# Kernel tuning notes

Measured on AMD Instinct MI355X. Metric: run time of the kernel, lower is better.

## Reference

```python
import jax, jax.numpy as jnp
import numpy as np
from jax import lax

NK = 21   # num_kernels / predicted kernel size
MK = 21   # max_kernel_size
B, H, W = 8, 256, 256


def _make_gauss_weight():
    """Fixed bank: identity kernel + 21 FFT-inverse gaussian kernels, repeated x3 channels."""
    def gauss1d(ws, sigma):
        xs = np.arange(ws)
        g = np.exp(-(xs - ws // 2) ** 2 / (2.0 * sigma ** 2))
        return g / g.sum()

    def inv_kernel(ws, sigma):
        g = gauss1d(ws, sigma)
        w2 = np.outer(g, g)
        K = np.fft.fft2(w2)
        K = np.conj(K) / (np.abs(K) ** 2 + 0.01)
        return np.abs(np.fft.ifft2(K))

    w = np.zeros((NK + 1, 1, MK, MK), np.float32)
    ks = 3
    for i in range(NK):
        pad = (MK - ks) // 2
        w[i + 1, 0, pad:pad + ks, pad:pad + ks] = inv_kernel(ks, 0.25 * (i + 1))
        if i >= 2 and i % 2 == 0 and ks < MK:
            ks += 2
    w[0, 0, MK // 2, MK // 2] = 1.0  # identity (delta) kernel
    return np.repeat(w, 3, axis=0)   # (66, 1, 21, 21)


def conv(x, w, pad, groups=1, b=None):
    y = lax.conv_general_dilated(
        x, w, (1, 1), [(pad, pad), (pad, pad)],
        dimension_numbers=("NCHW", "OIHW", "NCHW"),
        feature_group_count=groups)
    if b is not None:
        y = y + b[None, :, None, None]
    return y


def adaptive_avg_pool(x, oh, ow):
    """Matches torch AdaptiveAvgPool2d bin boundaries (static shapes)."""
    Hh, Ww = x.shape[2], x.shape[3]
    def bins(L, o):
        return [((i * L) // o, -((-(i + 1) * L) // o)) for i in range(o)]
    rows = []
    for (hs, he) in bins(Hh, oh):
        cols = [x[:, :, hs:he, ws:we].mean(axis=(2, 3)) for (ws, we) in bins(Ww, ow)]
        rows.append(jnp.stack(cols, axis=-1))
    return jnp.stack(rows, axis=-2)  # (N, C, oh, ow)


def setup_inputs() -> dict:
    key = jax.random.key(0)
    ks = jax.random.split(key, 12)
    s = 0.02
    return {
        "x": jax.random.normal(ks[0], (B, 3, H, W), jnp.float32),
        "w_gauss": jnp.asarray(_make_gauss_weight()),
        "p1_w": jax.random.normal(ks[1], (128, 3, 11, 11), jnp.float32) * s,
        "p1_b": jax.random.normal(ks[2], (128,), jnp.float32) * s,
        "p2_w": jax.random.normal(ks[3], (441, 128, 1, 1), jnp.float32) * s,
        "p3_w": jax.random.normal(ks[4], (441, 441, 1, 1), jnp.float32) * s,
        "cs_w": jax.random.normal(ks[5], (3, 3, 3, 3), jnp.float32) * s,
        "cs_b": jax.random.normal(ks[6], (3,), jnp.float32) * s,
        "tr_w": jax.random.normal(ks[7], (66, 3, 3, 3), jnp.float32) * s,
        "tr_b": jax.random.normal(ks[8], (66,), jnp.float32) * s,
        "fu_w": jax.random.normal(ks[9], (66, 132, 3, 3), jnp.float32) * s,
        "fu_b": jax.random.normal(ks[10], (66,), jnp.float32) * s,
    }


def reference(x, w_gauss, p1_w, p1_b, p2_w, p3_w, cs_w, cs_b, tr_w, tr_b, fu_w, fu_b):
    b = x.shape[0]
    pad = (NK - 1) // 2  # 10

    # fixed inverse-gaussian blur bank, grouped over the 3 input channels -> (B,66,H,W)
    x_gauss = conv(x, w_gauss, pad, groups=3)

    # Predictor: per-sample 3x21x21 dynamic kernel
    h = jax.nn.leaky_relu(conv(x, p1_w, 2, b=p1_b), 0.2)
    h = adaptive_avg_pool(h, 3, 3)
    h = jax.nn.leaky_relu(conv(h, p2_w, 0), 0.2)
    h = adaptive_avg_pool(h, 3, 1)           # (B,441,3,1)
    h = jax.nn.softmax(conv(h, p3_w, 0), axis=1)
    kern = h.reshape(b, 3, NK, NK)           # per-sample predicted kernel

    # batched per-sample dynamic conv: groups=B trick replaces the python loop
    xr = x.reshape(1, b * 3, x.shape[2], x.shape[3])
    out = conv(xr, kern, pad, groups=b)      # (1,B,H,W)
    output = jnp.broadcast_to(out.reshape(b, 1, x.shape[2], x.shape[3]), x.shape)

    ax_out = conv(x, cs_w, 1, b=cs_b)                       # (B,3,H,W)
    x_af = conv(output, tr_w, 1, b=tr_b)                    # (B,66,H,W)
    fused = conv(jnp.concatenate([x_gauss, x_af], axis=1), fu_w, 1, b=fu_b)  # (B,66,H,W)
    return (fused, ax_out)
```

## Files before the change

### kernel.cpp

```cpp
#include <hip/hip_runtime.h>
#include <hip/hip_bf16.h>

#define BB 8
#define HH 256
#define WW 256
#define HW 65536

typedef __attribute__((ext_vector_type(8))) short bf16x8;
typedef __attribute__((ext_vector_type(4))) float f32x4;
typedef __attribute__((ext_vector_type(8))) unsigned short u16x8;
#define MFMA16(a, b, c) __builtin_amdgcn_mfma_f32_16x16x32_bf16(a, b, c, 0, 0, 0)

__device__ __forceinline__ ushort f2bf(float f) {
  union { float f; uint32_t u; } c; c.f = f;
  uint32_t r = (c.u + 0x7fffu + ((c.u >> 16) & 1u)) >> 16;
  return (ushort)r;
}

#define OFF_XG    0
#define OFF_PP    25165824
#define OFF_XGN   69206016
#define OFF_OUT1  144703488
#define OFF_KERN  146837504
#define OFF_BW    146880000
#define OFF_BWZ   147018240
#define OFF_BP    147028480
#define OFF_BIAS  147126784
#define OFF_TB    147127296
#define OFF_T     147129856

__global__ __launch_bounds__(256) void k_prepA(const float* __restrict__ fuw,
                                               const float* __restrict__ trw,
                                               const float* __restrict__ trb,
                                               const float* __restrict__ p1w,
                                               float* __restrict__ T,
                                               float* __restrict__ TB,
                                               ushort* __restrict__ Bw,
                                               ushort* __restrict__ Bp) {
  int i = blockIdx.x * 256 + threadIdx.x;
  if (i < 5346) {
    int o = i / 81, a = (i / 9) % 9, s = i % 9;
    float acc = 0.f;
    for (int cp = 0; cp < 66; ++cp)
      acc += fuw[(o * 132 + 66 + cp) * 9 + a] *
             (trw[(cp * 3) * 9 + s] + trw[(cp * 3 + 1) * 9 + s] + trw[(cp * 3 + 2) * 9 + s]);
    T[i] = acc; return;
  }
  i -= 5346;
  if (i < 594) {
    int o = i / 9, a = i % 9;
    float acc = 0.f;
    for (int cp = 0; cp < 66; ++cp) acc += trb[cp] * fuw[(o * 132 + 66 + cp) * 9 + a];
    TB[i] = acc; return;
  }
  i -= 594;
  if (i < 2 * 9 * 80 * 32) {
    int cc = i / 23040, t = (i / 2560) % 9, o = (i / 32) % 80, kl = i & 31;
    int c = cc * 32 + kl;
    Bw[i] = (o < 66) ? f2bf(fuw[(o * 132 + c) * 9 + t]) : 0;
    return;
  }
  i -= 2 * 9 * 80 * 32;
  if (i < 12 * 128 * 32) {
    int kc = i / 4096, o = (i / 32) % 128, kl = i & 31;
    int k = kc * 32 + kl;
    float v = 0.f;
    if (k < 363) { int u = k / 33, r2 = k % 33, vv = r2 / 3, c = r2 % 3;
                   v = p1w[(o * 3 + c) * 121 + u * 11 + vv]; }
    Bp[i] = f2bf(v);
    return;
  }
}

__device__ __forceinline__ float W5val(int o, int d, const float* T) {
  int dy = d / 5, dx = d % 5;
  float acc = 0.f;
  for (int ua = 0; ua < 3; ++ua) {
    int us = dy - ua; if (us < 0 || us > 2) continue;
    for (int va = 0; va < 3; ++va) {
      int vs = dx - va; if (vs < 0 || vs > 2) continue;
      acc += T[(o * 9 + ua * 3 + va) * 9 + us * 3 + vs];
    }
  }
  return acc;
}

__global__ __launch_bounds__(256) void k_prepB(const float* __restrict__ fuw,
                                               const float* __restrict__ fub,
                                               const float* __restrict__ T,
                                               const float* __restrict__ TB,
                                               ushort* __restrict__ BwZ,
                                               float* __restrict__ bias_tot) {
  int i = blockIdx.x * 256 + threadIdx.x;
  if (i < 5120) {
    int zc = i / 2560, o = (i / 32) % 80, s = i & 31;
    float v = 0.f;
    if (o < 66) {
      if (zc == 0) {
        if (s < 18) { int ch = 64 + s / 9, a = s % 9; v = fuw[(o * 132 + ch) * 9 + a]; }
        else        { v = W5val(o, s - 18, T); }
      } else {
        if (s < 11) v = W5val(o, 14 + s, T);
      }
    }
    BwZ[i] = f2bf(v); return;
  }
  i -= 5120;
  if (i < 80) {
    float v = 0.f;
    if (i < 66) { v = fub[i]; for (int a = 0; a < 9; ++a) v += TB[i * 9 + a]; }
    bias_tot[i] = v;
  }
}

template <int KS>
__device__ __forceinline__ void xg_conv(const float* __restrict__ xt,
                                        const float* __restrict__ wgp,
                                        float* a, int r, int wq) {
  constexpr int P0 = (21 - KS) / 2;
  constexpr int Q0 = P0 & ~3;
  constexpr int D0 = P0 - Q0;
  constexpr int NL = ((P0 + KS + 6) >> 2) - (P0 >> 2) + 1;
#pragma unroll 1
  for (int kh = P0; kh < P0 + KS; ++kh) {
    float rx[NL * 4];
    const int F0 = (r + kh) * 320 + 8 * wq + Q0;
#pragma unroll
    for (int i = 0; i < NL; ++i) {
      int Fi = F0 + 4 * i;
      *(float4*)(rx + 4 * i) = *(const float4*)(xt + (Fi ^ (((Fi >> 5) & 1) << 2)));
    }
    const float* wr = wgp + kh * 21 + P0;
#pragma unroll
    for (int t = 0; t < KS; ++t) {
      float wv = wr[t];
#pragma unroll
      for (int u = 0; u < 8; ++u) a[u] += wv * rx[D0 + t + u];
    }
  }
}

__global__ __launch_bounds__(256, 4) void k_xgauss(const float* __restrict__ x,
                                                   const float* __restrict__ wg,
                                                   __hip_bfloat16* __restrict__ xg) {
  const int bu = blockIdx.z;
  const int b = bu / 24, u = bu % 24;
  const int g = u >> 3;
  const int j = (u & 7) + 7 * g;
  const int h0 = blockIdx.y * 8;
  __shared__ __align__(16) float xt[28 * 320];
  const float* xp = x + (b * 3 + g) * HW;
  for (int e = threadIdx.x; e < 28 * 320; e += 256) {
    int row = e / 320, col = e % 320;
    int gy = h0 + row - 10, gx = col - 10;
    float v = (gy >= 0 && gy < HH && gx >= 0 && gx < WW) ? xp[gy * WW + gx] : 0.f;
    xt[e ^ (((e >> 5) & 1) << 2)] = v;
  }
  __syncthreads();
  int i_ = j - 1;
  int im = (i_ - 1 > 0) ? (i_ - 1) : 0;
  const int ks = (j == 0) ? 1 : 3 + 2 * (im >> 1);
  const int wq = threadIdx.x & 31, r = threadIdx.x >> 5;
  const float* wgp = wg + (3 * j) * 441;
  float a[8] = {0.f, 0.f, 0.f, 0.f, 0.f, 0.f, 0.f, 0.f};
  switch (ks) {
    case 1:  xg_conv<1>(xt, wgp, a, r, wq); break;
    case 3:  xg_conv<3>(xt, wgp, a, r, wq); break;
    case 5:  xg_conv<5>(xt, wgp, a, r, wq); break;
    case 7:  xg_conv<7>(xt, wgp, a, r, wq); break;
    case 9:  xg_conv<9>(xt, wgp, a, r, wq); break;
    case 11: xg_conv<11>(xt, wgp, a, r, wq); break;
    case 13: xg_conv<13>(xt, wgp, a, r, wq); break;
    case 15: xg_conv<15>(xt, wgp, a, r, wq); break;
    case 17: xg_conv<17>(xt, wgp, a, r, wq); break;
    case 19: xg_conv<19>(xt, wgp, a, r, wq); break;
    default: xg_conv<21>(xt, wgp, a, r, wq); break;
  }
  u16x8 ov;
#pragma unroll
  for (int k = 0; k < 8; ++k) ov[k] = f2bf(a[k]);
  int oidx = (bu * HW) + (h0 + r) * WW + 8 * wq;
  *(u16x8*)((ushort*)xg + oidx) = ov;
}

__global__ __launch_bounds__(256) void k_tr(const ushort* __restrict__ xg,
                                            ushort* __restrict__ xgn) {
  __shared__ ushort ls[64 * 72];
  int p0 = blockIdx.x * 64;
  int b = p0 >> 16, sp = p0 & 65535;
  for (int e = threadIdx.x; e < 72 * 64; e += 256) {
    int c = e >> 6, i = e & 63;
    int uc = c / 3 + c / 22;
    ls[i * 72 + c] = (c < 66) ? xg[(size_t)(b * 24 + uc) * HW + sp + i] : (ushort)0;
  }
  __syncthreads();
  for (int e = threadIdx.x; e < 576; e += 256) {
    *(float4*)(xgn + (size_t)p0 * 72 + e * 8) = *(const float4*)(ls + e * 8);
  }
}

__global__ __launch_bounds__(256, 2) void k_pmm(const float* __restrict__ x,
                                                const ushort* __restrict__ Bp,
                                                const float* __restrict__ p1b,
                                                float* __restrict__ pp) {
  __shared__ float xt[26 * 26 * 3];
  __shared__ float ps[1152];
  const int b = blockIdx.z, h0 = blockIdx.y * 16, w0 = blockIdx.x * 16;
  const int tid = threadIdx.x, wave = tid >> 6, lane = tid & 63;
  const int m = lane & 15, q = lane >> 4;
  for (int e = tid; e < 1152; e += 256) ps[e] = 0.f;
  for (int e = tid; e < 676; e += 256) {
    int py = e / 26, pxc = e % 26, gy = h0 - 2 + py, gx = w0 - 2 + pxc;
    bool in = (gy >= 0 && gy < HH && gx >= 0 && gx < WW);
#pragma unroll
    for (int c = 0; c < 3; ++c)
      xt[e * 3 + c] = in ? x[(b * 3 + c) * HW + gy * WW + gx] : 0.f;
  }
  f32x4 acc[4][8];
#pragma unroll
  for (int a = 0; a < 4; ++a)
#pragma unroll
    for (int n = 0; n < 8; ++n) acc[a][n] = (f32x4){0.f, 0.f, 0.f, 0.f};
  __syncthreads();
  const int q8 = q * 8;
#pragma unroll
  for (int kc = 0; kc < 12; ++kc) {
    bf16x8 bf[8];
#pragma unroll
    for (int nt = 0; nt < 8; ++nt)
      bf[nt] = *(const bf16x8*)(Bp + ((kc * 128 + nt * 16 + m) * 32 + q8));
    int off[8];
#pragma unroll
    for (int j = 0; j < 8; ++j) {
      int k = kc * 32 + q8 + j;
      int kk = (kc == 11) ? (k > 362 ? 362 : k) : k;
      off[j] = kk + (kk / 33) * 45;
    }
#pragma unroll
    for (int mt = 0; mt < 4; ++mt) {
      const int row = (wave << 2) + mt;
      const int pb = (row * 26 + m) * 3;
      union { ushort us[8]; bf16x8 v; } af;
#pragma unroll
      for (int j = 0; j < 8; ++j) {
        ushort bvv = f2bf(xt[pb + off[j]]);
        if (kc == 11) {
          int k = kc * 32 + q8 + j;
          bvv = (k < 363) ? bvv : (ushort)0;
        }
        af.us[j] = bvv;
      }
#pragma unroll
      for (int nt = 0; nt < 8; ++nt)
        acc[mt][nt] = MFMA16(af.v, bf[nt], acc[mt][nt]);
    }
  }
  float bv[8];
#pragma unroll
  for (int nt = 0; nt < 8; ++nt) bv[nt] = p1b[nt * 16 + m];
#pragma unroll
  for (int mt = 0; mt < 4; ++mt) {
    int h = h0 + (wave << 2) + mt;
    if (h >= 250) continue;
    bool h0m = h < 84, h1m = (h >= 83 && h < 167), h2m = h >= 166;
#pragma unroll
    for (int r = 0; r < 4; ++r) {
      int w = w0 + (q << 2) + r;
      if (w >= 250) continue;
      bool w0m = w < 84, w1m = (w >= 83 && w < 167), w2m = w >= 166;
#pragma unroll
      for (int nt = 0; nt < 8; ++nt) {
        int o = (nt << 4) + m;
        float vz = acc[mt][nt][r] + bv[nt];
        vz = vz >= 0.f ? vz : 0.2f * vz;
        if (h0m) { if (w0m) atomicAdd(&ps[o], vz);        if (w1m) atomicAdd(&ps[128 + o], vz);
                   if (w2m) atomicAdd(&ps[256 + o], vz); }
        if (h1m) { if (w0m) atomicAdd(&ps[384 + o], vz);  if (w1m) atomicAdd(&ps[512 + o], vz);
                   if (w2m) atomicAdd(&ps[640 + o], vz); }
        if (h2m) { if (w0m) atomicAdd(&ps[768 + o], vz);  if (w1m) atomicAdd(&ps[896 + o], vz);
                   if (w2m) atomicAdd(&ps[1024 + o], vz); }
      }
    }
  }
  __syncthreads();
  const int tile = blockIdx.y * 16 + blockIdx.x;
  float* dst = pp + (size_t)(b * 256 + tile) * 1152;
  for (int e = tid; e < 1152; e += 256)
    dst[e] = ps[(e % 9) * 128 + (e / 9)];
}

__global__ __launch_bounds__(256) void k_pred2(const float* __restrict__ pp,
                                               const float* __restrict__ p2w,
                                               const float* __restrict__ p3w,
                                               float* __restrict__ kernw) {
  const int b = blockIdx.x;
  const int tid = threadIdx.x;
  __shared__ float hin[1152];
  __shared__ float h2p[1323];
  __shared__ float h3l[1323];
  __shared__ float mx[3], sm[3];
  for (int e = tid; e < 1152; e += 256) {
    float s = 0.f;
    const float* qp = pp + (size_t)b * 256 * 1152 + e;
#pragma unroll 4
    for (int t = 0; t < 256; ++t) s += qp[t * 1152];
    hin[e] = s * (1.f / 7056.f);
  }
  __syncthreads();
  for (int c = tid; c < 441; c += 256) {
    float z[9] = {0.f,0.f,0.f,0.f,0.f,0.f,0.f,0.f,0.f};
    const float* wr = p2w + c * 128;
    for (int k = 0; k < 128; k++) {
      float wv = wr[k];
      const float* hp = &hin[k * 9];
#pragma unroll
      for (int p = 0; p < 9; p++) z[p] += wv * hp[p];
    }
#pragma unroll
    for (int i = 0; i < 3; i++) {
      float s = 0.f;
#pragma unroll
      for (int jj = 0; jj < 3; jj++) {
        float zz = z[i * 3 + jj];
        s += (zz >= 0.f) ? zz : 0.2f * zz;
      }
      h2p[c * 3 + i] = s * (1.f / 3.f);
    }
  }
  __syncthreads();
  for (int c = tid; c < 441; c += 256) {
    float a0 = 0.f, a1 = 0.f, a2 = 0.f;
    const float* wr = p3w + c * 441;
    for (int k = 0; k < 441; k++) {
      float wv = wr[k];
      a0 += wv * h2p[k * 3];
      a1 += wv * h2p[k * 3 + 1];
      a2 += wv * h2p[k * 3 + 2];
    }
    h3l[c * 3] = a0; h3l[c * 3 + 1] = a1; h3l[c * 3 + 2] = a2;
  }
  __syncthreads();
  if (tid < 3) {
    float mxv = -1e30f;
    for (int c = 0; c < 441; c++) mxv = fmaxf(mxv, h3l[c * 3 + tid]);
    float s = 0.f;
    for (int c = 0; c < 441; c++) s += expf(h3l[c * 3 + tid] - mxv);
    mx[tid] = mxv; sm[tid] = 1.f / s;
  }
  __syncthreads();
  for (int f = tid; f < 1323; f += 256) {
    int i = f % 3;
    kernw[b * 1323 + f] = expf(h3l[f] - mx[i]) * sm[i];
  }
}

__global__ __launch_bounds__(256) void k_dyn(const float* __restrict__ x,
                                             const float* __restrict__ kernw,
                                             float* __restrict__ out1) {
  const int b = blockIdx.z;
  const int h0 = blockIdx.y * 16, w0 = blockIdx.x * 64;
  __shared__ float kl[1323];
  __shared__ float xt[3 * 36 * 84];
  for (int e = threadIdx.x; e < 1323; e += 256) kl[e] = kernw[b * 1323 + e];
  for (int e = threadIdx.x; e < 3 * 36 * 84; e += 256) {
    int ci = e / 3024, rem = e % 3024;
    int ty = rem / 84, tx = rem % 84;
    int gy = h0 + ty - 10, gx = w0 + tx - 10;
    xt[e] = (gy >= 0 && gy < HH && gx >= 0 && gx < WW)
                ? x[(b * 3 + ci) * HW + gy * WW + gx] : 0.f;
  }
  __syncthreads();
  const int wq = threadIdx.x & 15, r = threadIdx.x >> 4;
  float a0 = 0.f, a1 = 0.f, a2 = 0.f, a3 = 0.f;
  for (int ci = 0; ci < 3; ci++) {
    for (int kh = 0; kh < 21; kh++) {
      float rx[24];
      const float4* rp = (const float4*)&xt[ci * 3024 + (r + kh) * 84 + 4 * wq];
      float4* rv = (float4*)rx;
#pragma unroll
      for (int i = 0; i < 6; i++) rv[i] = rp[i];
      const float* wr = &kl[ci * 441 + kh * 21];
#pragma unroll
      for (int kw = 0; kw < 21; kw++) {
        float wv = wr[kw];
        a0 += wv * rx[kw];     a1 += wv * rx[kw + 1];
        a2 += wv * rx[kw + 2]; a3 += wv * rx[kw + 3];
      }
    }
  }
  int idx = b * HW + (h0 + r) * WW + w0 + 4 * wq;
  *(float4*)&out1[idx] = make_float4(a0, a1, a2, a3);
}

__global__ __launch_bounds__(256) void k_ax(const float* __restrict__ x,
                                            const float* __restrict__ csw,
                                            const float* __restrict__ csb,
                                            float* __restrict__ out2) {
  int idx = blockIdx.x * 256 + threadIdx.x;
  if (idx >= BB * 3 * HW) return;
  int w = idx & 255, h = (idx >> 8) & 255;
  int oc = (idx >> 16) % 3, b = idx / (3 * HW);
  float acc = csb[oc];
  for (int ic = 0; ic < 3; ic++) {
    const float* xc = x + (b * 3 + ic) * HW;
    const float* wp = csw + (oc * 3 + ic) * 9;
#pragma unroll
    for (int u = 0; u < 3; u++) {
      int iy = h + u - 1;
      if (iy < 0 || iy >= HH) continue;
#pragma unroll
      for (int v = 0; v < 3; v++) {
        int ix = w + v - 1;
        if (ix >= 0 && ix < WW) acc += xc[iy * WW + ix] * wp[u * 3 + v];
      }
    }
  }
  out2[idx] = acc;
}

__global__ __launch_bounds__(256, 3) void k_fmma(const ushort* __restrict__ xgn,
                                                 const float* __restrict__ out1,
                                                 const ushort* __restrict__ Bw,
                                                 const ushort* __restrict__ BwZ,
                                                 const float* __restrict__ bias_tot,
                                                 float* __restrict__ outf) {
  __shared__ __align__(16) char smem[40080];
  ushort* xs  = (ushort*)smem;
  float*  o1s = (float*)(smem + 20736);
  ushort* xs2 = (ushort*)(smem + 22336);
  ushort* az  = (ushort*)(smem + 23632);
  float*  st  = (float*)(smem + 23632);
  const int b = blockIdx.z, h0 = blockIdx.y * 16, w0 = blockIdx.x * 16;
  const int tid = threadIdx.x, wave = tid >> 6, lane = tid & 63;
  const int m = lane & 15, q = lane >> 4;
  f32x4 acc[4][5];
#pragma unroll
  for (int a = 0; a < 4; ++a)
#pragma unroll
    for (int n = 0; n < 5; ++n) acc[a][n] = (f32x4){0.f, 0.f, 0.f, 0.f};

  for (int cc = 0; cc < 2; ++cc) {
    __syncthreads();
    for (int e = tid; e < 1296; e += 256) {
      int u = e & 3, p = e >> 2, py = p / 18, px = p % 18;
      int gy = h0 - 1 + py, gx = w0 - 1 + px;
      float4 v = make_float4(0.f, 0.f, 0.f, 0.f);
      if (gy >= 0 && gy < HH && gx >= 0 && gx < WW)
        v = *(const float4*)(xgn + (size_t)(b * HW + gy * WW + gx) * 72 + cc * 32 + u * 8);
      *(float4*)(xs + p * 32 + u * 8) = v;
    }
    __syncthreads();
#pragma unroll
    for (int t = 0; t < 9; ++t) {
      const int u = t / 3, v = t % 3;
      bf16x8 bf[5];
#pragma unroll
      for (int nt = 0; nt < 5; ++nt)
        bf[nt] = *(const bf16x8*)(Bw + (((cc * 9 + t) * 80 + nt * 16 + m) * 32 + q * 8));
#pragma unroll
      for (int mt = 0; mt < 4; ++mt) {
        int row = (wave << 2) + mt;
        bf16x8 af = *(const bf16x8*)(xs + ((row + u) * 18 + m + v) * 32 + q * 8);
#pragma unroll
        for (int nt = 0; nt < 5; ++nt)
          acc[mt][nt] = MFMA16(af, bf[nt], acc[mt][nt]);
      }
    }
  }
  __syncthreads();
  for (int e = tid; e < 324; e += 256) {
    int py = e / 18, px = e % 18, gy = h0 - 1 + py, gx = w0 - 1 + px;
    uint32_t v = 0;
    if (gy >= 0 && gy < HH && gx >= 0 && gx < WW)
      v = *(const uint32_t*)(xgn + (size_t)(b * HW + gy * WW + gx) * 72 + 64);
    *(uint32_t*)(xs2 + e * 2) = v;
  }
  for (int e = tid; e < 400; e += 256) {
    int py = e / 20, px = e % 20, gy = h0 - 2 + py, gx = w0 - 2 + px;
    o1s[e] = (gy >= 0 && gy < HH && gx >= 0 && gx < WW) ? out1[b * HW + gy * WW + gx] : 0.f;
  }
  __syncthreads();
  const int bpy = tid >> 4, bpx = tid & 15;
#pragma unroll
  for (int zc = 0; zc < 2; ++zc) {
    union { ushort us[32]; float4 f4[4]; } vals;
    if (zc == 0) {
#pragma unroll
      for (int s = 0; s < 18; ++s) {
        int ch = s / 9, a = s % 9, u = a / 3, v = a % 3;
        vals.us[s] = xs2[((bpy + u) * 18 + bpx + v) * 2 + ch];
      }
#pragma unroll
      for (int d = 0; d < 14; ++d)
        vals.us[18 + d] = f2bf(o1s[(bpy + d / 5) * 20 + bpx + d % 5]);
    } else {
#pragma unroll
      for (int s = 0; s < 11; ++s) {
        int d = 14 + s;
        vals.us[s] = f2bf(o1s[(bpy + d / 5) * 20 + bpx + d % 5]);
      }
#pragma unroll
      for (int s = 11; s < 32; ++s) vals.us[s] = 0;
    }
    __syncthreads();
#pragma unroll
    for (int u = 0; u < 4; ++u)
      *(float4*)(az + tid * 32 + ((u ^ (tid & 3)) << 3)) = vals.f4[u];
    __syncthreads();
    bf16x8 bf[5];
#pragma unroll
    for (int nt = 0; nt < 5; ++nt)
      bf[nt] = *(const bf16x8*)(BwZ + ((zc * 80 + nt * 16 + m) * 32 + q * 8));
#pragma unroll
    for (int mt = 0; mt < 4; ++mt) {
      int px = (((wave << 2) + mt) << 4) + m;
      bf16x8 af = *(const bf16x8*)(az + px * 32 + ((q ^ (px & 3)) << 3));
#pragma unroll
      for (int nt = 0; nt < 5; ++nt)
        acc[mt][nt] = MFMA16(af, bf[nt], acc[mt][nt]);
    }
  }
#pragma unroll 1
  for (int nt = 0; nt < 5; ++nt) {
    __syncthreads();
#pragma unroll
    for (int mt = 0; mt < 4; ++mt) {
      int pxb = (((wave << 2) + mt) << 4);
#pragma unroll
      for (int r = 0; r < 4; ++r)
        st[m * 257 + pxb + q * 4 + r] = acc[mt][nt][r];
    }
    __syncthreads();
#pragma unroll
    for (int kk = 0; kk < 16; ++kk) {
      int o = nt * 16 + kk;
      if (o < 66) {
        float bvv = bias_tot[o];
        outf[((b * 66 + o) * HH + h0 + (tid >> 4)) * WW + w0 + (tid & 15)] =
            st[kk * 257 + tid] + bvv;
      }
    }
  }
}

__global__ __launch_bounds__(256) void k_fix(const float* __restrict__ out1,
                                             const float* __restrict__ T,
                                             const float* __restrict__ TB,
                                             float* __restrict__ outf) {
  int idx = blockIdx.x * 256 + threadIdx.x;
  if (idx >= 8 * 1020 * 66) return;
  int b = idx / (1020 * 66);
  int rem = idx % (1020 * 66);
  int pi = rem / 66, o = rem % 66;
  int ph, pw;
  if (pi < 256)      { ph = 0;        pw = pi; }
  else if (pi < 512) { ph = 255;      pw = pi - 256; }
  else if (pi < 766) { ph = pi - 511; pw = 0; }
  else               { ph = pi - 765; pw = 255; }
  float corr = 0.f;
#pragma unroll
  for (int a = 0; a < 9; ++a) {
    int ua = a / 3, va = a % 3;
    int qh = ph + ua - 1, qw = pw + va - 1;
    if (qh >= 0 && qh < HH && qw >= 0 && qw < WW) continue;
    float s = TB[o * 9 + a];
#pragma unroll
    for (int t2 = 0; t2 < 9; ++t2) {
      int rh = qh + t2 / 3 - 1, rw = qw + t2 % 3 - 1;
      if (rh >= 0 && rh < HH && rw >= 0 && rw < WW)
        s += out1[b * HW + rh * WW + rw] * T[(o * 9 + a) * 9 + t2];
    }
    corr += s;
  }
  outf[((b * 66 + o) * HH + ph) * WW + pw] -= corr;
}

extern "C" void kernel_launch(void* const* d_in, const int* in_sizes, int n_in,
                              void* d_out, int out_size, void* d_ws, size_t ws_size,
                              hipStream_t stream) {
  const float* x   = (const float*)d_in[0];
  const float* wg  = (const float*)d_in[1];
  const float* p1w = (const float*)d_in[2];
  const float* p1b = (const float*)d_in[3];
  const float* p2w = (const float*)d_in[4];
  const float* p3w = (const float*)d_in[5];
  const float* csw = (const float*)d_in[6];
  const float* csb = (const float*)d_in[7];
  const float* trw = (const float*)d_in[8];
  const float* trb = (const float*)d_in[9];
  const float* fuw = (const float*)d_in[10];
  const float* fub = (const float*)d_in[11];
  float* outf = (float*)d_out;
  float* out2 = outf + 34603008;
  char* ws = (char*)d_ws;
  __hip_bfloat16* xg = (__hip_bfloat16*)(ws + OFF_XG);
  float* pp      = (float*)(ws + OFF_PP);
  ushort* xgn    = (ushort*)(ws + OFF_XGN);
  float* out1    = (float*)(ws + OFF_OUT1);
  float* kernw   = (float*)(ws + OFF_KERN);
  ushort* Bw     = (ushort*)(ws + OFF_BW);
  ushort* BwZ    = (ushort*)(ws + OFF_BWZ);
  ushort* Bp     = (ushort*)(ws + OFF_BP);
  float* biasT   = (float*)(ws + OFF_BIAS);
  float* TBp     = (float*)(ws + OFF_TB);
  float* Tp      = (float*)(ws + OFF_T);

  hipLaunchKernelGGL(k_prepA, dim3(397), dim3(256), 0, stream,
                     fuw, trw, trb, p1w, Tp, TBp, Bw, Bp);
  hipLaunchKernelGGL(k_prepB, dim3(21), dim3(256), 0, stream,
                     fuw, fub, Tp, TBp, BwZ, biasT);
  hipLaunchKernelGGL(k_xgauss, dim3(1, 32, 8 * 24), dim3(256), 0, stream, x, wg, xg);
  hipLaunchKernelGGL(k_tr, dim3(8192), dim3(256), 0, stream, (const ushort*)xg, xgn);
  hipLaunchKernelGGL(k_pmm, dim3(16, 16, 8), dim3(256), 0, stream, x, Bp, p1b, pp);
  hipLaunchKernelGGL(k_pred2, dim3(8), dim3(256), 0, stream, pp, p2w, p3w, kernw);
  hipLaunchKernelGGL(k_dyn, dim3(4, 16, 8), dim3(256), 0, stream, x, kernw, out1);
  hipLaunchKernelGGL(k_fmma, dim3(16, 16, 8), dim3(256), 0, stream,
                     xgn, out1, Bw, BwZ, biasT, outf);
  hipLaunchKernelGGL(k_fix, dim3(2104), dim3(256), 0, stream, out1, Tp, TBp, outf);
  hipLaunchKernelGGL(k_ax, dim3(6144), dim3(256), 0, stream, x, csw, csb, out2);
}
```

Baseline: 1.335 ms.

## Pad predictor conv im2col to 4-channel layout and quadruple k_pmm threads

Stores the k_pmm input tile with 4 channels per pixel (the fourth zero) and re-lays out the 11x11 weight matrix to K=484. Each A fragment can then be read with two float4 LDS loads instead of eight scalar gathers with index arithmetic. The block grows to 1024 threads with one 16-pixel row per wave, and shared-memory atomics are spread across four per-quad partial buffers that are summed at the end. This adds about 33% more MFMA work for the zero padding and changes occupancy and register pressure.

```diff
diff --git a/kernel.cpp b/kernel.cpp
--- a/kernel.cpp
+++ b/kernel.cpp
@@ -19,12 +19,12 @@
 
 #define OFF_XG    0
 #define OFF_PP    25165824
+#define OFF_BP    34603008
 #define OFF_XGN   69206016
 #define OFF_OUT1  144703488
 #define OFF_KERN  146837504
 #define OFF_BW    146880000
 #define OFF_BWZ   147018240
-#define OFF_BP    147028480
 #define OFF_BIAS  147126784
 #define OFF_TB    147127296
 #define OFF_T     147129856
@@ -61,12 +61,12 @@
     return;
   }
   i -= 2 * 9 * 80 * 32;
-  if (i < 12 * 128 * 32) {
+  if (i < 16 * 128 * 32) {
     int kc = i / 4096, o = (i / 32) % 128, kl = i & 31;
     int k = kc * 32 + kl;
     float v = 0.f;
-    if (k < 363) { int u = k / 33, r2 = k % 33, vv = r2 / 3, c = r2 % 3;
-                   v = p1w[(o * 3 + c) * 121 + u * 11 + vv]; }
+    if (k < 484) { int u = k / 44, r2 = k % 44, vv = r2 / 4, c = r2 & 3;
+                   if (c < 3) v = p1w[(o * 3 + c) * 121 + u * 11 + vv]; }
     Bp[i] = f2bf(v);
     return;
   }
@@ -199,69 +199,60 @@
   }
 }
 
-__global__ __launch_bounds__(256, 2) void k_pmm(const float* __restrict__ x,
-                                                const ushort* __restrict__ Bp,
-                                                const float* __restrict__ p1b,
-                                                float* __restrict__ pp) {
-  __shared__ float xt[26 * 26 * 3];
-  __shared__ float ps[1152];
+__global__ __launch_bounds__(1024, 4) void k_pmm(const float* __restrict__ x,
+                                                 const ushort* __restrict__ Bp,
+                                                 const float* __restrict__ p1b,
+                                                 float* __restrict__ pp) {
+  __shared__ __align__(16) float xt2[3840];
+  __shared__ float ps[4 * 1152];
   const int b = blockIdx.z, h0 = blockIdx.y * 16, w0 = blockIdx.x * 16;
   const int tid = threadIdx.x, wave = tid >> 6, lane = tid & 63;
   const int m = lane & 15, q = lane >> 4;
-  for (int e = tid; e < 1152; e += 256) ps[e] = 0.f;
-  for (int e = tid; e < 676; e += 256) {
-    int py = e / 26, pxc = e % 26, gy = h0 - 2 + py, gx = w0 - 2 + pxc;
-    bool in = (gy >= 0 && gy < HH && gx >= 0 && gx < WW);
-#pragma unroll
-    for (int c = 0; c < 3; ++c)
-      xt[e * 3 + c] = in ? x[(b * 3 + c) * HW + gy * WW + gx] : 0.f;
-  }
-  f32x4 acc[4][8];
-#pragma unroll
-  for (int a = 0; a < 4; ++a)
-#pragma unroll
-    for (int n = 0; n < 8; ++n) acc[a][n] = (f32x4){0.f, 0.f, 0.f, 0.f};
+  for (int e = tid; e < 4608; e += 1024) ps[e] = 0.f;
+  if (tid < 676) {
+    int py = tid / 26, pxc = tid % 26, gy = h0 - 2 + py, gx = w0 - 2 + pxc;
+    float4 v = make_float4(0.f, 0.f, 0.f, 0.f);
+    if (gy >= 0 && gy < HH && gx >= 0 && gx < WW) {
+      const float* xb = x + b * 3 * HW + gy * WW + gx;
+      v.x = xb[0]; v.y = xb[HW]; v.z = xb[2 * HW];
+    }
+    *(float4*)(xt2 + tid * 4) = v;
+  }
+  for (int e = tid; e < 1136; e += 1024) xt2[2704 + e] = 0.f;
+  f32x4 acc[8];
+#pragma unroll
+  for (int n = 0; n < 8; ++n) acc[n] = (f32x4){0.f, 0.f, 0.f, 0.f};
   __syncthreads();
   const int q8 = q * 8;
-#pragma unroll
-  for (int kc = 0; kc < 12; ++kc) {
+  const float* afb = xt2 + (wave * 26 + m) * 4;
+#pragma unroll
+  for (int kc = 0; kc < 16; ++kc) {
+    const int s = kc * 32 + q8;
+    const int u = (s * 745) >> 15;
+    const int rem = s - 44 * u;
+    const int a0 = s + 60 * u;
+    const int a1 = a0 + ((rem == 40) ? 64 : 4);
+    float4 lo = *(const float4*)(afb + a0);
+    float4 hi = *(const float4*)(afb + a1);
+    union { ushort us[8]; bf16x8 v; } af;
+    af.us[0] = f2bf(lo.x); af.us[1] = f2bf(lo.y);
+    af.us[2] = f2bf(lo.z); af.us[3] = f2bf(lo.w);
+    af.us[4] = f2bf(hi.x); af.us[5] = f2bf(hi.y);
+    af.us[6] = f2bf(hi.z); af.us[7] = f2bf(hi.w);
     bf16x8 bf[8];
 #pragma unroll
     for (int nt = 0; nt < 8; ++nt)
       bf[nt] = *(const bf16x8*)(Bp + ((kc * 128 + nt * 16 + m) * 32 + q8));
-    int off[8];
-#pragma unroll
-    for (int j = 0; j < 8; ++j) {
-      int k = kc * 32 + q8 + j;
-      int kk = (kc == 11) ? (k > 362 ? 362 : k) : k;
-      off[j] = kk + (kk / 33) * 45;
-    }
-#pragma unroll
-    for (int mt = 0; mt < 4; ++mt) {
-      const int row = (wave << 2) + mt;
-      const int pb = (row * 26 + m) * 3;
-      union { ushort us[8]; bf16x8 v; } af;
-#pragma unroll
-      for (int j = 0; j < 8; ++j) {
-        ushort bvv = f2bf(xt[pb + off[j]]);
-        if (kc == 11) {
-          int k = kc * 32 + q8 + j;
-          bvv = (k < 363) ? bvv : (ushort)0;
-        }
-        af.us[j] = bvv;
-      }
-#pragma unroll
-      for (int nt = 0; nt < 8; ++nt)
-        acc[mt][nt] = MFMA16(af.v, bf[nt], acc[mt][nt]);
-    }
+#pragma unroll
+    for (int nt = 0; nt < 8; ++nt)
+      acc[nt] = MFMA16(af.v, bf[nt], acc[nt]);
   }
   float bv[8];
 #pragma unroll
   for (int nt = 0; nt < 8; ++nt) bv[nt] = p1b[nt * 16 + m];
-#pragma unroll
-  for (int mt = 0; mt < 4; ++mt) {
-    int h = h0 + (wave << 2) + mt;
-    if (h >= 250) continue;
+  const int h = h0 + wave;
+  float* psq = ps + q * 1152;
+  if (h < 250) {
     bool h0m = h < 84, h1m = (h >= 83 && h < 167), h2m = h >= 166;
 #pragma unroll
     for (int r = 0; r < 4; ++r) {
@@ -271,22 +262,24 @@
 #pragma unroll
       for (int nt = 0; nt < 8; ++nt) {
         int o = (nt << 4) + m;
-        float vz = acc[mt][nt][r] + bv[nt];
+        float vz = acc[nt][r] + bv[nt];
         vz = vz >= 0.f ? vz : 0.2f * vz;
-        if (h0m) { if (w0m) atomicAdd(&ps[o], vz);        if (w1m) atomicAdd(&ps[128 + o], vz);
-                   if (w2m) atomicAdd(&ps[256 + o], vz); }
-        if (h1m) { if (w0m) atomicAdd(&ps[384 + o], vz);  if (w1m) atomicAdd(&ps[512 + o], vz);
-                   if (w2m) atomicAdd(&ps[640 + o], vz); }
-        if (h2m) { if (w0m) atomicAdd(&ps[768 + o], vz);  if (w1m) atomicAdd(&ps[896 + o], vz);
-                   if (w2m) atomicAdd(&ps[1024 + o], vz); }
+        if (h0m) { if (w0m) atomicAdd(&psq[o], vz);        if (w1m) atomicAdd(&psq[128 + o], vz);
+                   if (w2m) atomicAdd(&psq[256 + o], vz); }
+        if (h1m) { if (w0m) atomicAdd(&psq[384 + o], vz);  if (w1m) atomicAdd(&psq[512 + o], vz);
+                   if (w2m) atomicAdd(&psq[640 + o], vz); }
+        if (h2m) { if (w0m) atomicAdd(&psq[768 + o], vz);  if (w1m) atomicAdd(&psq[896 + o], vz);
+                   if (w2m) atomicAdd(&psq[1024 + o], vz); }
       }
     }
   }
   __syncthreads();
   const int tile = blockIdx.y * 16 + blockIdx.x;
   float* dst = pp + (size_t)(b * 256 + tile) * 1152;
-  for (int e = tid; e < 1152; e += 256)
-    dst[e] = ps[(e % 9) * 128 + (e / 9)];
+  for (int e = tid; e < 1152; e += 1024) {
+    int idx = (e % 9) * 128 + (e / 9);
+    dst[e] = ps[idx] + ps[1152 + idx] + ps[2304 + idx] + ps[3456 + idx];
+  }
 }
 
 __global__ __launch_bounds__(256) void k_pred2(const float* __restrict__ pp,
@@ -595,23 +588,23 @@
   char* ws = (char*)d_ws;
   __hip_bfloat16* xg = (__hip_bfloat16*)(ws + OFF_XG);
   float* pp      = (float*)(ws + OFF_PP);
+  ushort* Bp     = (ushort*)(ws + OFF_BP);
   ushort* xgn    = (ushort*)(ws + OFF_XGN);
   float* out1    = (float*)(ws + OFF_OUT1);
   float* kernw   = (float*)(ws + OFF_KERN);
   ushort* Bw     = (ushort*)(ws + OFF_BW);
   ushort* BwZ    = (ushort*)(ws + OFF_BWZ);
-  ushort* Bp     = (ushort*)(ws + OFF_BP);
   float* biasT   = (float*)(ws + OFF_BIAS);
   float* TBp     = (float*)(ws + OFF_TB);
   float* Tp      = (float*)(ws + OFF_T);
 
-  hipLaunchKernelGGL(k_prepA, dim3(397), dim3(256), 0, stream,
+  hipLaunchKernelGGL(k_prepA, dim3(460), dim3(256), 0, stream,
                      fuw, trw, trb, p1w, Tp, TBp, Bw, Bp);
   hipLaunchKernelGGL(k_prepB, dim3(21), dim3(256), 0, stream,
                      fuw, fub, Tp, TBp, BwZ, biasT);
   hipLaunchKernelGGL(k_xgauss, dim3(1, 32, 8 * 24), dim3(256), 0, stream, x, wg, xg);
   hipLaunchKernelGGL(k_tr, dim3(8192), dim3(256), 0, stream, (const ushort*)xg, xgn);
-  hipLaunchKernelGGL(k_pmm, dim3(16, 16, 8), dim3(256), 0, stream, x, Bp, p1b, pp);
+  hipLaunchKernelGGL(k_pmm, dim3(16, 16, 8), dim3(1024), 0, stream, x, Bp, p1b, pp);
   hipLaunchKernelGGL(k_pred2, dim3(8), dim3(256), 0, stream, pp, p2w, p3w, kernw);
   hipLaunchKernelGGL(k_dyn, dim3(4, 16, 8), dim3(256), 0, stream, x, kernw, out1);
   hipLaunchKernelGGL(k_fmma, dim3(16, 16, 8), dim3(256), 0, stream,
```

Result: slower. 1.499 ms (+12.3%).
